# Optimization experiments

Hardware: AMD Instinct MI355X
Metric: run time of the kernel (lower is better)

The kernel has to match this reference:

```python
import jax, jax.numpy as jnp
import numpy as np

EPS = 1e-5
NUM_HEADS = 8
NUM_GROUPS = 32


def conv1x1(x, w, b):
    # x: [B,C,H,W], w: [O,C], b: [O]
    return jnp.einsum('bchw,oc->bohw', x, w) + b[None, :, None, None]


def group_norm(x, w, b, groups=NUM_GROUPS, eps=EPS):
    B, C, H, W = x.shape
    xg = x.reshape(B, groups, C // groups, H, W)
    mean = xg.mean(axis=(2, 3, 4), keepdims=True)
    var = xg.var(axis=(2, 3, 4), keepdims=True)
    xn = ((xg - mean) * jax.lax.rsqrt(var + eps)).reshape(B, C, H, W)
    return xn * w[None, :, None, None] + b[None, :, None, None]


def setup_inputs() -> dict:
    key = jax.random.key(0)
    ks = jax.random.split(key, 12)
    B, C, H, W = 2, 256, 64, 64
    inner = C  # head_dim * num_heads = 32 * 8
    s = 1.0 / np.sqrt(C)
    return {
        'query_feat': jax.random.normal(ks[0], (B, C, H, W), jnp.float32),
        'key_feat': jax.random.normal(ks[1], (B, C, H, W), jnp.float32),
        'q_w': jax.random.normal(ks[2], (inner, C), jnp.float32) * s,
        'q_b': jnp.zeros((inner,), jnp.float32),
        'k_w': jax.random.normal(ks[3], (inner, C), jnp.float32) * s,
        'k_b': jnp.zeros((inner,), jnp.float32),
        'v_w': jax.random.normal(ks[4], (inner, C), jnp.float32) * s,
        'v_b': jnp.zeros((inner,), jnp.float32),
        'out_w': jax.random.normal(ks[5], (C, inner), jnp.float32) * s,
        'out_b': jnp.zeros((C,), jnp.float32),
        'gn_w': jnp.ones((C,), jnp.float32),
        'gn_b': jnp.zeros((C,), jnp.float32),
    }


def reference(query_feat, key_feat, q_w, q_b, k_w, k_b, v_w, v_b, out_w, out_b, gn_w, gn_b):
    B, C, H, W = query_feat.shape
    N = H * W
    h = NUM_HEADS
    d = C // h
    # 1x1 conv projections, then [B, h, N, d]
    def heads(x):
        return x.reshape(B, h, d, N).transpose(0, 1, 3, 2)
    Q = heads(conv1x1(query_feat, q_w, q_b))
    K = heads(conv1x1(key_feat, k_w, k_b))
    V = heads(conv1x1(key_feat, v_w, v_b))
    scores = jnp.einsum('bhnd,bhmd->bhnm', Q, K) * (d ** -0.5)  # [B,h,N,N]
    attn = jax.nn.softmax(scores, axis=-1)
    out = jnp.einsum('bhnm,bhmd->bhnd', attn, V)  # [B,h,N,d]
    out = out.transpose(0, 1, 3, 2).reshape(B, h * d, H, W)
    proj = conv1x1(out, out_w, out_b)
    return group_norm(query_feat + proj, gn_w, gn_b)
```

## Files before the change

kernel.cpp:

```cpp
#include <hip/hip_runtime.h>
#include <math.h>

#define C_DIM 256
#define N_DIM 4096
#define NHEAD 8

using bf16x8 = __attribute__((ext_vector_type(8))) short;
using f32x16 = __attribute__((ext_vector_type(16))) float;

__device__ __forceinline__ short f32_to_bf16(float a) {
    return (short)((__float_as_uint(a) + 0x8000u) >> 16);
}
__device__ __forceinline__ float bf16_to_f32(unsigned short u) {
    return __uint_as_float(((unsigned)u) << 16);
}
__device__ __forceinline__ unsigned pack_trunc(float a, float b) {
    return __builtin_amdgcn_perm(__float_as_uint(b), __float_as_uint(a), 0x07060302u);
}

__device__ __forceinline__ int SWZ(int m, int c) {
    return (m >> 5) * 8192 + (c >> 4) * 512 + ((c >> 3) & 1) * 256 + (m & 31) * 8 + (c & 7);
}

__global__ __launch_bounds__(256) void prep(
    const float* __restrict__ query, const float* __restrict__ key,
    const float* __restrict__ qw, const float* __restrict__ kw,
    const float* __restrict__ vw, const float* __restrict__ ow,
    short* __restrict__ Qx, short* __restrict__ Kx, short* __restrict__ Wsw,
    float* __restrict__ gstats)
{
    const int t = threadIdx.x;
    if (blockIdx.z == 4) {
        const int p = blockIdx.y;
        if (blockIdx.x == 0 && p == 0 && t < 128) gstats[t] = 0.f;
        const float* src = (p == 0) ? qw : (p == 1) ? kw : (p == 2) ? vw : ow;
        const int idx = (blockIdx.x * 256 + t) * 4;
        const int o = idx >> 8, c = idx & 255;
        float4 v = *(const float4*)&src[idx];
        short* dst = Wsw + p * 65536 + SWZ(o, c);
        dst[0] = f32_to_bf16(v.x); dst[1] = f32_to_bf16(v.y);
        dst[2] = f32_to_bf16(v.z); dst[3] = f32_to_bf16(v.w);
        return;
    }
    __shared__ short Ts[64][72];
    const int z = blockIdx.z;
    const float* in = (z < 2) ? query : key;
    short* out = ((z < 2) ? Qx : Kx) + (size_t)(z & 1) * N_DIM * C_DIM;
    const size_t ibase = (size_t)(z & 1) * C_DIM * N_DIM;
    const int n0 = blockIdx.x * 64, c0 = blockIdx.y * 64;
    const int cl = t >> 4, nl4 = (t & 15) * 4;
#pragma unroll
    for (int p = 0; p < 4; ++p) {
        const int c = cl + p * 16;
        float4 v = *(const float4*)&in[ibase + (size_t)(c0 + c) * N_DIM + n0 + nl4];
        Ts[nl4 + 0][c] = f32_to_bf16(v.x);
        Ts[nl4 + 1][c] = f32_to_bf16(v.y);
        Ts[nl4 + 2][c] = f32_to_bf16(v.z);
        Ts[nl4 + 3][c] = f32_to_bf16(v.w);
    }
    __syncthreads();
    const int nl = t >> 3, cg = t & 7;
#pragma unroll
    for (int half = 0; half < 2; ++half) {
        const int nloc = nl + half * 32;
        const int c = c0 + cg * 8;
        uint4 val = *(const uint4*)&Ts[nloc][cg * 8];
        *(uint4*)&out[SWZ(n0 + nloc, c)] = val;
    }
}

__global__ __launch_bounds__(256) void qkv_gemm(
    const short* __restrict__ Wsw, const short* __restrict__ Qx,
    const short* __restrict__ Kx,
    const float* __restrict__ q_b, const float* __restrict__ k_b,
    const float* __restrict__ v_b,
    short* __restrict__ Qt, short* __restrict__ Kt, short* __restrict__ Vt,
    float qscale)
{
    const int t = threadIdx.x, w = t >> 6, lane = t & 63;
    const int q2 = lane >> 5, l31 = lane & 31;
    const int proj = blockIdx.z >> 1, b = blockIdx.z & 1;
    const int n0 = blockIdx.x * 64 + (w >> 1) * 32;
    const int o0 = blockIdx.y * 64 + (w & 1) * 32;
    const short* X = ((proj == 0) ? Qx : Kx) + (size_t)b * N_DIM * C_DIM;
    const short* W = Wsw + proj * 65536;
    const float* bias = (proj == 0) ? q_b : (proj == 1) ? k_b : v_b;
    const int xbase = (n0 >> 5) * 8192 + q2 * 256 + l31 * 8;
    const int wbase = (o0 >> 5) * 8192 + q2 * 256 + l31 * 8;

    f32x16 acc;
#pragma unroll
    for (int r = 0; r < 16; ++r) acc[r] = 0.f;

#pragma unroll 4
    for (int kc = 0; kc < C_DIM; kc += 16) {
        bf16x8 xf = *(const bf16x8*)&X[xbase + (kc >> 4) * 512];
        bf16x8 wf = *(const bf16x8*)&W[wbase + (kc >> 4) * 512];
        if (proj == 2)
            acc = __builtin_amdgcn_mfma_f32_32x32x16_bf16(wf, xf, acc, 0, 0, 0);
        else
            acc = __builtin_amdgcn_mfma_f32_32x32x16_bf16(xf, wf, acc, 0, 0, 0);
    }

    const int head = o0 >> 5;
    if (proj < 2) {
        short* OH = ((proj == 0) ? Qt : Kt) + (size_t)(b * NHEAD + head) * N_DIM * 32;
        const float bi = bias[o0 + l31];
        const float sc = (proj == 0) ? qscale : 1.f;
        const int cbase = (n0 >> 5) * 1024 + (l31 >> 4) * 512 + ((l31 >> 3) & 1) * 256 + (l31 & 7);
#pragma unroll
        for (int r = 0; r < 16; ++r) {
            const int qs = (r & 3) + 8 * (r >> 2) + 4 * q2;
            OH[cbase + qs * 8] = f32_to_bf16((acc[r] + bi) * sc);
        }
    } else {
        short* VH = Vt + (size_t)(b * NHEAD + head) * N_DIM * 32;
        const int kbase = (n0 >> 5) * 1024 + (l31 >> 4) * 512 + ((l31 >> 3) & 1) * 256 + (l31 & 7);
#pragma unroll
        for (int r = 0; r < 16; ++r) {
            const int ds = (r & 3) + 8 * (r >> 2) + 4 * q2;
            VH[kbase + ds * 8] = f32_to_bf16(acc[r] + bias[o0 + ds]);
        }
    }
}

__global__ __launch_bounds__(256) void flash_mfma(
    const short* __restrict__ Qt, const short* __restrict__ Kt,
    const short* __restrict__ Vt, short* __restrict__ Opart,
    float* __restrict__ lpart)
{
    const int n0 = blockIdx.x * 128;
    const int h  = blockIdx.y;
    const int z  = blockIdx.z;
    const int b  = z >> 2, s = z & 3;
    const int CHUNK = N_DIM / 4;
    const int t = threadIdx.x, w = t >> 6, lane = t & 63;
    const int q2 = lane >> 5, l31 = lane & 31;
    const int q  = n0 + w * 32 + l31;
    const int bhp = b * NHEAD + h;
    const size_t hb = (size_t)bhp * N_DIM * 32;

    const int qoff = (q >> 5) * 1024 + q2 * 256 + (q & 31) * 8;
    bf16x8 Qf0 = *(const bf16x8*)&Qt[hb + qoff];
    bf16x8 Qf1 = *(const bf16x8*)&Qt[hb + qoff + 512];

    int off = ((s * CHUNK) >> 5) * 1024 + q2 * 256 + l31 * 8;
    bf16x8 Kc0 = *(const bf16x8*)&Kt[hb + off];
    bf16x8 Kc1 = *(const bf16x8*)&Kt[hb + off + 512];
    bf16x8 Vc0 = *(const bf16x8*)&Vt[hb + off];
    bf16x8 Vc1 = *(const bf16x8*)&Vt[hb + off + 512];
    off += 1024;

    f32x16 Of;
#pragma unroll
    for (int r = 0; r < 16; ++r) Of[r] = 0.f;
    float ls = 0.f;

    for (int it = 0; it < CHUNK / 32; ++it) {
        bf16x8 Kn0 = *(const bf16x8*)&Kt[hb + off];
        bf16x8 Kn1 = *(const bf16x8*)&Kt[hb + off + 512];
        bf16x8 Vn0 = *(const bf16x8*)&Vt[hb + off];
        bf16x8 Vn1 = *(const bf16x8*)&Vt[hb + off + 512];
        off += 1024;

        f32x16 acc;
#pragma unroll
        for (int r = 0; r < 16; ++r) acc[r] = 0.f;
        acc = __builtin_amdgcn_mfma_f32_32x32x16_bf16(Kc0, Qf0, acc, 0, 0, 0);
        acc = __builtin_amdgcn_mfma_f32_32x32x16_bf16(Kc1, Qf1, acc, 0, 0, 0);

        float p[16];
#pragma unroll
        for (int r = 0; r < 16; ++r) { p[r] = __builtin_amdgcn_exp2f(acc[r]); ls += p[r]; }

        unsigned u[8], xu[8];
#pragma unroll
        for (int g = 0; g < 8; ++g) u[g] = pack_trunc(p[2 * g], p[2 * g + 1]);
#pragma unroll
        for (int g = 0; g < 8; ++g) xu[g] = (unsigned)__shfl_xor((int)u[g], 32, 64);

        uint4 f0, f1;
        f0.x = q2 ? xu[2] : u[0];  f0.y = q2 ? xu[3] : u[1];
        f0.z = q2 ? u[2]  : xu[0]; f0.w = q2 ? u[3]  : xu[1];
        f1.x = q2 ? xu[6] : u[4];  f1.y = q2 ? xu[7] : u[5];
        f1.z = q2 ? u[6]  : xu[4]; f1.w = q2 ? u[7]  : xu[5];
        bf16x8 Pf0 = __builtin_bit_cast(bf16x8, f0);
        bf16x8 Pf1 = __builtin_bit_cast(bf16x8, f1);

        Of = __builtin_amdgcn_mfma_f32_32x32x16_bf16(Vc0, Pf0, Of, 0, 0, 0);
        Of = __builtin_amdgcn_mfma_f32_32x32x16_bf16(Vc1, Pf1, Of, 0, 0, 0);

        Kc0 = Kn0; Kc1 = Kn1; Vc0 = Vn0; Vc1 = Vn1;
    }

    ls += __shfl_xor(ls, 32, 64);

    const size_t obase = ((size_t)(s * 16 + bhp) * N_DIM + q) * 32;
#pragma unroll
    for (int g = 0; g < 4; ++g) {
        ushort4 st;
        st.x = (unsigned short)f32_to_bf16(Of[4 * g + 0]);
        st.y = (unsigned short)f32_to_bf16(Of[4 * g + 1]);
        st.z = (unsigned short)f32_to_bf16(Of[4 * g + 2]);
        st.w = (unsigned short)f32_to_bf16(Of[4 * g + 3]);
        *(ushort4*)&Opart[obase + 8 * g + 4 * q2] = st;
    }
    lpart[(size_t)(s * 16 + bhp) * N_DIM + q] = ls;
}

__global__ __launch_bounds__(256) void combine4(
    const short* __restrict__ Opart, const float* __restrict__ lpart,
    short* __restrict__ AOt)
{
    const int n0 = blockIdx.x * 64;
    const int p  = blockIdx.y;
    const int bb = p >> 3, hh = p & 7;
    const int t = threadIdx.x;
    __shared__ float linv[64];

    if (t < 64) {
        float sum = 0.f;
#pragma unroll
        for (int s = 0; s < 4; ++s)
            sum += lpart[(size_t)(s * 16 + p) * N_DIM + n0 + t];
        linv[t] = 1.f / sum;
    }
    __syncthreads();

    const int nl = t >> 2;
    const int dg = (t & 3) * 8;
    float a[8];
#pragma unroll
    for (int j = 0; j < 8; ++j) a[j] = 0.f;
#pragma unroll
    for (int s = 0; s < 4; ++s) {
        const size_t rb = ((size_t)(s * 16 + p) * N_DIM + n0 + nl) * 32 + dg;
        ushort4 u0 = *(const ushort4*)&Opart[rb];
        ushort4 u1 = *(const ushort4*)&Opart[rb + 4];
        a[0] += bf16_to_f32(u0.x); a[1] += bf16_to_f32(u0.y);
        a[2] += bf16_to_f32(u0.z); a[3] += bf16_to_f32(u0.w);
        a[4] += bf16_to_f32(u1.x); a[5] += bf16_to_f32(u1.y);
        a[6] += bf16_to_f32(u1.z); a[7] += bf16_to_f32(u1.w);
    }
    const float rl = linv[nl];
    ushort4 o0v, o1v;
    o0v.x = (unsigned short)f32_to_bf16(a[0] * rl);
    o0v.y = (unsigned short)f32_to_bf16(a[1] * rl);
    o0v.z = (unsigned short)f32_to_bf16(a[2] * rl);
    o0v.w = (unsigned short)f32_to_bf16(a[3] * rl);
    o1v.x = (unsigned short)f32_to_bf16(a[4] * rl);
    o1v.y = (unsigned short)f32_to_bf16(a[5] * rl);
    o1v.z = (unsigned short)f32_to_bf16(a[6] * rl);
    o1v.w = (unsigned short)f32_to_bf16(a[7] * rl);
    short* dst = &AOt[(size_t)bb * N_DIM * C_DIM + SWZ(n0 + nl, hh * 32 + dg)];
    *(ushort4*)dst = o0v;
    *(ushort4*)(dst + 4) = o1v;
}

__global__ __launch_bounds__(256) void out_gemm(
    const short* __restrict__ OWsw, const short* __restrict__ AOt,
    const float* __restrict__ ob, const float* __restrict__ query,
    short* __restrict__ y16)
{
    const int t = threadIdx.x, w = t >> 6, lane = t & 63;
    const int q2 = lane >> 5, l31 = lane & 31;
    const int n0 = blockIdx.x * 32, o0 = blockIdx.y * 32, b = blockIdx.z;
    const short* B = AOt + (size_t)b * N_DIM * C_DIM;
    const int abase = (o0 >> 5) * 8192 + q2 * 256 + l31 * 8;
    const int bbase = (n0 >> 5) * 8192 + q2 * 256 + l31 * 8;

    f32x16 acc;
#pragma unroll
    for (int r = 0; r < 16; ++r) acc[r] = 0.f;

    const int kc0 = w * 64;
#pragma unroll
    for (int s2 = 0; s2 < 4; ++s2) {
        const int kc = kc0 + s2 * 16;
        bf16x8 af = *(const bf16x8*)&OWsw[abase + (kc >> 4) * 512];
        bf16x8 bf = *(const bf16x8*)&B[bbase + (kc >> 4) * 512];
        acc = __builtin_amdgcn_mfma_f32_32x32x16_bf16(af, bf, acc, 0, 0, 0);
    }

    __shared__ float red[3][64][17];
    if (w > 0) {
#pragma unroll
        for (int r = 0; r < 16; ++r) red[w - 1][lane][r] = acc[r];
    }
    __syncthreads();
    if (w == 0) {
#pragma unroll
        for (int r = 0; r < 16; ++r)
            acc[r] += red[0][lane][r] + red[1][lane][r] + red[2][lane][r];
        const size_t base = (size_t)b * C_DIM * N_DIM;
#pragma unroll
        for (int r = 0; r < 16; ++r) {
            const int o = o0 + (r & 3) + 8 * (r >> 2) + 4 * q2;
            const int n = n0 + l31;
            const size_t addr = base + (size_t)o * N_DIM + n;
            y16[addr] = f32_to_bf16(acc[r] + ob[o] + query[addr]);
        }
    }
}

__global__ __launch_bounds__(256) void gn_stats(
    const short* __restrict__ y16, float* __restrict__ gstats)
{
    const int g = blockIdx.x, b = blockIdx.y, sl = blockIdx.z;
    const size_t base = ((size_t)b * C_DIM + (size_t)g * 8) * N_DIM + sl * 1024;
    const int t = threadIdx.x;
    float sum = 0.f, sumsq = 0.f;
#pragma unroll
    for (int i = 0; i < 8; ++i) {
        const int idx = t + i * 256;
        const int row = idx >> 8, col = (idx & 255) * 4;
        ushort4 u = *(const ushort4*)&y16[base + (size_t)row * N_DIM + col];
        const float v0 = bf16_to_f32(u.x), v1 = bf16_to_f32(u.y);
        const float v2 = bf16_to_f32(u.z), v3 = bf16_to_f32(u.w);
        sum   += v0 + v1 + v2 + v3;
        sumsq += v0 * v0 + v1 * v1 + v2 * v2 + v3 * v3;
    }
#pragma unroll
    for (int off = 1; off < 64; off <<= 1) {
        sum   += __shfl_xor(sum, off, 64);
        sumsq += __shfl_xor(sumsq, off, 64);
    }
    __shared__ float red[8];
    const int wid = t >> 6;
    if ((t & 63) == 0) { red[wid] = sum; red[4 + wid] = sumsq; }
    __syncthreads();
    if (t == 0) {
        const int grp = b * 32 + g;
        atomicAdd(&gstats[grp * 2 + 0], red[0] + red[1] + red[2] + red[3]);
        atomicAdd(&gstats[grp * 2 + 1], red[4] + red[5] + red[6] + red[7]);
    }
}

__global__ __launch_bounds__(256) void gn_apply(
    const short* __restrict__ y16, const float* __restrict__ gstats,
    const float* __restrict__ gw, const float* __restrict__ gb,
    float* __restrict__ out)
{
    const int g = blockIdx.x, b = blockIdx.y, sl = blockIdx.z;
    const float s  = gstats[(b * 32 + g) * 2 + 0];
    const float qq = gstats[(b * 32 + g) * 2 + 1];
    const float mean = s * (1.f / 32768.f);
    const float var  = qq * (1.f / 32768.f) - mean * mean;
    const float rstd = rsqrtf(var + 1e-5f);

    const size_t base = ((size_t)b * C_DIM + (size_t)g * 8) * N_DIM + sl * 1024;
    const int t = threadIdx.x;
#pragma unroll
    for (int i = 0; i < 8; ++i) {
        const int idx = t + i * 256;
        const int row = idx >> 8, col = (idx & 255) * 4;
        const size_t a = base + (size_t)row * N_DIM + col;
        const float wv  = gw[g * 8 + row] * rstd;
        const float bb2 = gb[g * 8 + row];
        ushort4 u = *(const ushort4*)&y16[a];
        float4 v;
        v.x = (bf16_to_f32(u.x) - mean) * wv + bb2;
        v.y = (bf16_to_f32(u.y) - mean) * wv + bb2;
        v.z = (bf16_to_f32(u.z) - mean) * wv + bb2;
        v.w = (bf16_to_f32(u.w) - mean) * wv + bb2;
        *(float4*)&out[a] = v;
    }
}

extern "C" void kernel_launch(void* const* d_in, const int* in_sizes, int n_in,
                              void* d_out, int out_size, void* d_ws, size_t ws_size,
                              hipStream_t stream)
{
    const float* query = (const float*)d_in[0];
    const float* key   = (const float*)d_in[1];
    const float* q_w   = (const float*)d_in[2];
    const float* q_b   = (const float*)d_in[3];
    const float* k_w   = (const float*)d_in[4];
    const float* k_b   = (const float*)d_in[5];
    const float* v_w   = (const float*)d_in[6];
    const float* v_b   = (const float*)d_in[7];
    const float* o_w   = (const float*)d_in[8];
    const float* o_b   = (const float*)d_in[9];
    const float* gn_w  = (const float*)d_in[10];
    const float* gn_b  = (const float*)d_in[11];

    char* wsb = (char*)d_ws;
    short* Wsw   = (short*)wsb;
    float* gstats= (float*)(wsb + (3u << 18));
    short* Qx    = (short*)(wsb + (1u  << 20));
    short* Kx    = (short*)(wsb + (5u  << 20));
    short* Qt    = (short*)(wsb + (9u  << 20));
    short* Kt    = (short*)(wsb + (13u << 20));
    short* Vt    = (short*)(wsb + (17u << 20));
    short* Opart = (short*)(wsb + (21u << 20));
    float* lpart = (float*)(wsb + (37u << 20));
    short* AOt   = Qx;
    short* y16   = Opart;

    const float qscale = 0.17677669529663687f * 1.4426950408889634f;

    prep<<<dim3(64, 4, 5), 256, 0, stream>>>(query, key, q_w, k_w, v_w, o_w,
                                             Qx, Kx, Wsw, gstats);
    qkv_gemm<<<dim3(64, 4, 6), 256, 0, stream>>>(Wsw, Qx, Kx, q_b, k_b, v_b,
                                                 Qt, Kt, Vt, qscale);
    flash_mfma<<<dim3(32, 8, 8), 256, 0, stream>>>(Qt, Kt, Vt, Opart, lpart);
    combine4<<<dim3(64, 16), 256, 0, stream>>>(Opart, lpart, AOt);
    out_gemm<<<dim3(128, 8, 2), 256, 0, stream>>>(Wsw + 3 * 65536, AOt, o_b,
                                                  query, y16);
    gn_stats<<<dim3(32, 2, 4), 256, 0, stream>>>(y16, gstats);
    gn_apply<<<dim3(32, 2, 4), 256, 0, stream>>>(y16, gstats, gn_w, gn_b,
                                                 (float*)d_out);
}
```

Before: 175.3 us.

## Fuse split-KV combine into output GEMM and drop GN atomics

The split-KV partial outputs and softmax denominators are now reduced and normalized directly inside the output projection GEMM, which removes the separate combine kernel and its AOt round trip through memory. The output GEMM is restructured so each warp owns 32 output channels and runs the full K=256 reduction itself, with no LDS cross-warp reduction. The GroupNorm stats kernel now gives each group to one block and writes its result directly, so the zeroing in prep and the atomics are no longer needed. The prep transpose is also rewritten to pack bf16 pairs with rounding into a 32-bit LDS tile. The trade-off is that the GEMM reads four partial buffers per tile, and gn_stats runs with fewer blocks.

```diff
diff --git a/kernel.cpp b/kernel.cpp
--- a/kernel.cpp
+++ b/kernel.cpp
@@ -16,6 +16,10 @@
 }
 __device__ __forceinline__ unsigned pack_trunc(float a, float b) {
     return __builtin_amdgcn_perm(__float_as_uint(b), __float_as_uint(a), 0x07060302u);
+}
+__device__ __forceinline__ unsigned pack_rnd(float a, float b) {
+    return __builtin_amdgcn_perm(__float_as_uint(b) + 0x8000u,
+                                 __float_as_uint(a) + 0x8000u, 0x07060302u);
 }
 
 __device__ __forceinline__ int SWZ(int m, int c) {
@@ -26,13 +30,11 @@
     const float* __restrict__ query, const float* __restrict__ key,
     const float* __restrict__ qw, const float* __restrict__ kw,
     const float* __restrict__ vw, const float* __restrict__ ow,
-    short* __restrict__ Qx, short* __restrict__ Kx, short* __restrict__ Wsw,
-    float* __restrict__ gstats)
+    short* __restrict__ Qx, short* __restrict__ Kx, short* __restrict__ Wsw)
 {
     const int t = threadIdx.x;
     if (blockIdx.z == 4) {
         const int p = blockIdx.y;
-        if (blockIdx.x == 0 && p == 0 && t < 128) gstats[t] = 0.f;
         const float* src = (p == 0) ? qw : (p == 1) ? kw : (p == 2) ? vw : ow;
         const int idx = (blockIdx.x * 256 + t) * 4;
         const int o = idx >> 8, c = idx & 255;
@@ -42,30 +44,32 @@
         dst[2] = f32_to_bf16(v.z); dst[3] = f32_to_bf16(v.w);
         return;
     }
-    __shared__ short Ts[64][72];
+    __shared__ unsigned Ts32[32][33];
     const int z = blockIdx.z;
     const float* in = (z < 2) ? query : key;
     short* out = ((z < 2) ? Qx : Kx) + (size_t)(z & 1) * N_DIM * C_DIM;
     const size_t ibase = (size_t)(z & 1) * C_DIM * N_DIM;
     const int n0 = blockIdx.x * 64, c0 = blockIdx.y * 64;
-    const int cl = t >> 4, nl4 = (t & 15) * 4;
-#pragma unroll
-    for (int p = 0; p < 4; ++p) {
-        const int c = cl + p * 16;
-        float4 v = *(const float4*)&in[ibase + (size_t)(c0 + c) * N_DIM + n0 + nl4];
-        Ts[nl4 + 0][c] = f32_to_bf16(v.x);
-        Ts[nl4 + 1][c] = f32_to_bf16(v.y);
-        Ts[nl4 + 2][c] = f32_to_bf16(v.z);
-        Ts[nl4 + 3][c] = f32_to_bf16(v.w);
-    }
-    __syncthreads();
-    const int nl = t >> 3, cg = t & 7;
-#pragma unroll
-    for (int half = 0; half < 2; ++half) {
-        const int nloc = nl + half * 32;
-        const int c = c0 + cg * 8;
-        uint4 val = *(const uint4*)&Ts[nloc][cg * 8];
-        *(uint4*)&out[SWZ(n0 + nloc, c)] = val;
+    const int cp = t >> 3, ng = t & 7;
+
+#pragma unroll
+    for (int h2 = 0; h2 < 2; ++h2) {
+        const int nb = h2 * 32 + ng * 4;
+        float4 a = *(const float4*)&in[ibase + (size_t)(c0 + 2 * cp) * N_DIM + n0 + nb];
+        float4 b = *(const float4*)&in[ibase + (size_t)(c0 + 2 * cp + 1) * N_DIM + n0 + nb];
+        Ts32[ng * 4 + 0][cp] = pack_rnd(a.x, b.x);
+        Ts32[ng * 4 + 1][cp] = pack_rnd(a.y, b.y);
+        Ts32[ng * 4 + 2][cp] = pack_rnd(a.z, b.z);
+        Ts32[ng * 4 + 3][cp] = pack_rnd(a.w, b.w);
+        __syncthreads();
+        const int nl = t >> 3, cg = t & 7;
+        uint4 val;
+        val.x = Ts32[nl][cg * 4 + 0];
+        val.y = Ts32[nl][cg * 4 + 1];
+        val.z = Ts32[nl][cg * 4 + 2];
+        val.w = Ts32[nl][cg * 4 + 3];
+        *(uint4*)&out[SWZ(n0 + h2 * 32 + nl, c0 + cg * 8)] = val;
+        __syncthreads();
     }
 }
 
@@ -208,113 +212,80 @@
     lpart[(size_t)(s * 16 + bhp) * N_DIM + q] = ls;
 }
 
-__global__ __launch_bounds__(256) void combine4(
-    const short* __restrict__ Opart, const float* __restrict__ lpart,
-    short* __restrict__ AOt)
-{
-    const int n0 = blockIdx.x * 64;
-    const int p  = blockIdx.y;
-    const int bb = p >> 3, hh = p & 7;
-    const int t = threadIdx.x;
-    __shared__ float linv[64];
-
-    if (t < 64) {
-        float sum = 0.f;
-#pragma unroll
-        for (int s = 0; s < 4; ++s)
-            sum += lpart[(size_t)(s * 16 + p) * N_DIM + n0 + t];
-        linv[t] = 1.f / sum;
-    }
-    __syncthreads();
-
-    const int nl = t >> 2;
-    const int dg = (t & 3) * 8;
-    float a[8];
-#pragma unroll
-    for (int j = 0; j < 8; ++j) a[j] = 0.f;
-#pragma unroll
-    for (int s = 0; s < 4; ++s) {
-        const size_t rb = ((size_t)(s * 16 + p) * N_DIM + n0 + nl) * 32 + dg;
-        ushort4 u0 = *(const ushort4*)&Opart[rb];
-        ushort4 u1 = *(const ushort4*)&Opart[rb + 4];
-        a[0] += bf16_to_f32(u0.x); a[1] += bf16_to_f32(u0.y);
-        a[2] += bf16_to_f32(u0.z); a[3] += bf16_to_f32(u0.w);
-        a[4] += bf16_to_f32(u1.x); a[5] += bf16_to_f32(u1.y);
-        a[6] += bf16_to_f32(u1.z); a[7] += bf16_to_f32(u1.w);
-    }
-    const float rl = linv[nl];
-    ushort4 o0v, o1v;
-    o0v.x = (unsigned short)f32_to_bf16(a[0] * rl);
-    o0v.y = (unsigned short)f32_to_bf16(a[1] * rl);
-    o0v.z = (unsigned short)f32_to_bf16(a[2] * rl);
-    o0v.w = (unsigned short)f32_to_bf16(a[3] * rl);
-    o1v.x = (unsigned short)f32_to_bf16(a[4] * rl);
-    o1v.y = (unsigned short)f32_to_bf16(a[5] * rl);
-    o1v.z = (unsigned short)f32_to_bf16(a[6] * rl);
-    o1v.w = (unsigned short)f32_to_bf16(a[7] * rl);
-    short* dst = &AOt[(size_t)bb * N_DIM * C_DIM + SWZ(n0 + nl, hh * 32 + dg)];
-    *(ushort4*)dst = o0v;
-    *(ushort4*)(dst + 4) = o1v;
-}
-
 __global__ __launch_bounds__(256) void out_gemm(
-    const short* __restrict__ OWsw, const short* __restrict__ AOt,
-    const float* __restrict__ ob, const float* __restrict__ query,
-    short* __restrict__ y16)
+    const short* __restrict__ OWsw, const short* __restrict__ Opart,
+    const float* __restrict__ lpart, const float* __restrict__ ob,
+    const float* __restrict__ query, short* __restrict__ y16)
 {
     const int t = threadIdx.x, w = t >> 6, lane = t & 63;
     const int q2 = lane >> 5, l31 = lane & 31;
-    const int n0 = blockIdx.x * 32, o0 = blockIdx.y * 32, b = blockIdx.z;
-    const short* B = AOt + (size_t)b * N_DIM * C_DIM;
+    const int n0 = blockIdx.x * 32, b = blockIdx.y, oz = blockIdx.z;
+    const int o0 = oz * 128 + w * 32;
+    const int n = n0 + l31;
+
+    float linv[8];
+#pragma unroll
+    for (int h = 0; h < 8; ++h) {
+        float s = 0.f;
+#pragma unroll
+        for (int s4 = 0; s4 < 4; ++s4)
+            s += lpart[(size_t)(s4 * 16 + b * 8 + h) * N_DIM + n];
+        linv[h] = 1.f / s;
+    }
+
     const int abase = (o0 >> 5) * 8192 + q2 * 256 + l31 * 8;
-    const int bbase = (n0 >> 5) * 8192 + q2 * 256 + l31 * 8;
+    const size_t SSTR = (size_t)16 * N_DIM * 32;
 
     f32x16 acc;
 #pragma unroll
     for (int r = 0; r < 16; ++r) acc[r] = 0.f;
 
-    const int kc0 = w * 64;
-#pragma unroll
-    for (int s2 = 0; s2 < 4; ++s2) {
-        const int kc = kc0 + s2 * 16;
-        bf16x8 af = *(const bf16x8*)&OWsw[abase + (kc >> 4) * 512];
-        bf16x8 bf = *(const bf16x8*)&B[bbase + (kc >> 4) * 512];
-        acc = __builtin_amdgcn_mfma_f32_32x32x16_bf16(af, bf, acc, 0, 0, 0);
-    }
-
-    __shared__ float red[3][64][17];
-    if (w > 0) {
-#pragma unroll
-        for (int r = 0; r < 16; ++r) red[w - 1][lane][r] = acc[r];
-    }
-    __syncthreads();
-    if (w == 0) {
-#pragma unroll
-        for (int r = 0; r < 16; ++r)
-            acc[r] += red[0][lane][r] + red[1][lane][r] + red[2][lane][r];
-        const size_t base = (size_t)b * C_DIM * N_DIM;
-#pragma unroll
-        for (int r = 0; r < 16; ++r) {
-            const int o = o0 + (r & 3) + 8 * (r >> 2) + 4 * q2;
-            const int n = n0 + l31;
-            const size_t addr = base + (size_t)o * N_DIM + n;
-            y16[addr] = f32_to_bf16(acc[r] + ob[o] + query[addr]);
+#pragma unroll
+    for (int kc = 0; kc < 16; ++kc) {
+        const int head = kc >> 1;
+        const int d0 = (kc & 1) * 16 + q2 * 8;
+        const size_t base0 = ((size_t)(b * 8 + head) * N_DIM + n) * 32 + d0;
+        bf16x8 p0 = *(const bf16x8*)&Opart[base0];
+        bf16x8 p1 = *(const bf16x8*)&Opart[base0 + SSTR];
+        bf16x8 p2 = *(const bf16x8*)&Opart[base0 + 2 * SSTR];
+        bf16x8 p3 = *(const bf16x8*)&Opart[base0 + 3 * SSTR];
+        const float rl = linv[head];
+        float p[8];
+#pragma unroll
+        for (int j = 0; j < 8; ++j) {
+            p[j] = (bf16_to_f32((unsigned short)p0[j]) + bf16_to_f32((unsigned short)p1[j]) +
+                    bf16_to_f32((unsigned short)p2[j]) + bf16_to_f32((unsigned short)p3[j])) * rl;
         }
+        uint4 pk;
+        pk.x = pack_rnd(p[0], p[1]);
+        pk.y = pack_rnd(p[2], p[3]);
+        pk.z = pack_rnd(p[4], p[5]);
+        pk.w = pack_rnd(p[6], p[7]);
+        bf16x8 bfv = __builtin_bit_cast(bf16x8, pk);
+        bf16x8 af = *(const bf16x8*)&OWsw[abase + kc * 512];
+        acc = __builtin_amdgcn_mfma_f32_32x32x16_bf16(af, bfv, acc, 0, 0, 0);
+    }
+
+    const size_t base = (size_t)b * C_DIM * N_DIM;
+#pragma unroll
+    for (int r = 0; r < 16; ++r) {
+        const int o = o0 + (r & 3) + 8 * (r >> 2) + 4 * q2;
+        const size_t addr = base + (size_t)o * N_DIM + n;
+        y16[addr] = f32_to_bf16(acc[r] + ob[o] + query[addr]);
     }
 }
 
 __global__ __launch_bounds__(256) void gn_stats(
     const short* __restrict__ y16, float* __restrict__ gstats)
 {
-    const int g = blockIdx.x, b = blockIdx.y, sl = blockIdx.z;
-    const size_t base = ((size_t)b * C_DIM + (size_t)g * 8) * N_DIM + sl * 1024;
+    const int g = blockIdx.x, b = blockIdx.y;
+    const size_t base = ((size_t)b * C_DIM + (size_t)g * 8) * N_DIM;
     const int t = threadIdx.x;
     float sum = 0.f, sumsq = 0.f;
 #pragma unroll
-    for (int i = 0; i < 8; ++i) {
+    for (int i = 0; i < 32; ++i) {
         const int idx = t + i * 256;
-        const int row = idx >> 8, col = (idx & 255) * 4;
-        ushort4 u = *(const ushort4*)&y16[base + (size_t)row * N_DIM + col];
+        ushort4 u = *(const ushort4*)&y16[base + (size_t)idx * 4];
         const float v0 = bf16_to_f32(u.x), v1 = bf16_to_f32(u.y);
         const float v2 = bf16_to_f32(u.z), v3 = bf16_to_f32(u.w);
         sum   += v0 + v1 + v2 + v3;
@@ -331,8 +302,8 @@
     __syncthreads();
     if (t == 0) {
         const int grp = b * 32 + g;
-        atomicAdd(&gstats[grp * 2 + 0], red[0] + red[1] + red[2] + red[3]);
-        atomicAdd(&gstats[grp * 2 + 1], red[4] + red[5] + red[6] + red[7]);
+        gstats[grp * 2 + 0] = red[0] + red[1] + red[2] + red[3];
+        gstats[grp * 2 + 1] = red[4] + red[5] + red[6] + red[7];
     }
 }
 
@@ -394,20 +365,18 @@
     short* Vt    = (short*)(wsb + (17u << 20));
     short* Opart = (short*)(wsb + (21u << 20));
     float* lpart = (float*)(wsb + (37u << 20));
-    short* AOt   = Qx;
-    short* y16   = Opart;
+    short* y16   = Qx;
 
     const float qscale = 0.17677669529663687f * 1.4426950408889634f;
 
     prep<<<dim3(64, 4, 5), 256, 0, stream>>>(query, key, q_w, k_w, v_w, o_w,
-                                             Qx, Kx, Wsw, gstats);
+                                             Qx, Kx, Wsw);
     qkv_gemm<<<dim3(64, 4, 6), 256, 0, stream>>>(Wsw, Qx, Kx, q_b, k_b, v_b,
                                                  Qt, Kt, Vt, qscale);
     flash_mfma<<<dim3(32, 8, 8), 256, 0, stream>>>(Qt, Kt, Vt, Opart, lpart);
-    combine4<<<dim3(64, 16), 256, 0, stream>>>(Opart, lpart, AOt);
-    out_gemm<<<dim3(128, 8, 2), 256, 0, stream>>>(Wsw + 3 * 65536, AOt, o_b,
-                                                  query, y16);
-    gn_stats<<<dim3(32, 2, 4), 256, 0, stream>>>(y16, gstats);
+    out_gemm<<<dim3(128, 2, 2), 256, 0, stream>>>(Wsw + 3 * 65536, Opart, lpart,
+                                                  o_b, query, y16);
+    gn_stats<<<dim3(32, 2), 256, 0, stream>>>(y16, gstats);
     gn_apply<<<dim3(32, 2, 4), 256, 0, stream>>>(y16, gstats, gn_w, gn_b,
                                                  (float*)d_out);
 }
```

New measurement: 177.0 us. No clear change (+1.0%).
